# Kernel optimization log

Hardware: AMD Instinct MI355X
Metric: run time of the kernel (lower is better)

Reference implementation:

```python
import jax, jax.numpy as jnp
import numpy as np

NEG = 1e9  # large negative bias used by the original code for masked positions


def setup_inputs() -> dict:
    key = jax.random.key(0)
    k1, k2, k3 = jax.random.split(key, 3)
    B, H, W, Ck, Cv = 8, 64, 64, 64, 128
    return {
        "query": jax.random.normal(k1, (B, H, W, Ck), dtype=jnp.float32),
        "key": jax.random.normal(k2, (B, H, W, Ck), dtype=jnp.float32),
        "value": jax.random.normal(k3, (B, H, W, Cv), dtype=jnp.float32),
    }


def reference(query, key, value):
    B, Hq, Wq, Ck = query.shape
    Cv = value.shape[-1]
    Nq = Hq * Wq                      # query canvas size
    Nk = key.shape[1] * key.shape[2]  # key/value canvas size

    q = query.reshape(B, Nq, Ck)
    k = key.reshape(B, Nk, Ck)
    v = value.reshape(B, Nk, Cv)

    # strictly-causal pixelSNAIL mask: pixel i may attend only to pixels j < i
    allowed = jnp.tril(jnp.ones((Nq, Nk), dtype=query.dtype), k=-1)

    # [B, Nq, Nk] scaled dot-product scores
    scores = jnp.einsum("bqc,bkc->bqk", q, k) / jnp.sqrt(jnp.asarray(Ck, query.dtype))
    scores = scores - NEG * (1.0 - allowed)

    # softmax then redundant re-mask (as in the original module)
    probs = jax.nn.softmax(scores, axis=-1) * allowed

    out = jnp.einsum("bqk,bkv->bqv", probs, v)
    return out.reshape(B, Hq, Wq, Cv)
```

## Files before the change

kernel.cpp:

```cpp
#include <hip/hip_runtime.h>
#include <hip/hip_bf16.h>

typedef unsigned short u16;
typedef unsigned int u32;
typedef __attribute__((ext_vector_type(2))) unsigned int u32x2;
typedef __attribute__((ext_vector_type(4))) unsigned int u32x4;
typedef __attribute__((ext_vector_type(4))) float f32x4;
typedef __attribute__((ext_vector_type(8))) short bf16x8;
typedef __attribute__((ext_vector_type(16))) float f32x16;

__device__ __forceinline__ u32 cvtpk(float lo, float hi) {
    __hip_bfloat162 h = __float22bfloat162_rn(make_float2(lo, hi));
    u32 r; __builtin_memcpy(&r, &h, 4);
    return r;
}
__device__ __forceinline__ int crow(int r, int hl) { return (r & 3) + 8 * (r >> 2) + 4 * hl; }

#define NROW 4096
#define CK 64
#define CV 128
#define BUF 24576
#define VT_OFF 8192
#define SWK(R, o) ((((R) << 7) + (o)) ^ (((R) & 7) << 4))
#define SWVG(R) ((((R) >> 3) & 15) ^ (((R) & 7) << 1))
#define SWV(R, o) ((((R) << 8) + (o)) ^ (SWVG(R) << 4))

__global__ __launch_bounds__(512, 2) void attn_k(const float* __restrict__ Qg,
                                                 const float* __restrict__ Kg,
                                                 const float* __restrict__ Vg,
                                                 float* __restrict__ O) {
    __shared__ __align__(16) u16 smem[2 * BUF];

    int bid = blockIdx.x;
    int bb = bid & 7;
    int u  = bid >> 3;
    int t  = threadIdx.x;
    int w  = t >> 6;
    int lane = t & 63;
    int ql = lane & 31, hl = lane >> 5;
    int qsub = w >> 2;
    int jq   = w & 3;
    int uL = u, uH = 63 - u;
    int rA = ((2 * uL + 1) >> 2) + 1;

    const float* Qp = Qg + (size_t)bb * NROW * CK;
    const float* Kp = Kg + (size_t)bb * NROW * CK;
    const float* Vp = Vg + (size_t)bb * NROW * CV;
    const float qscale = 0.125f * 1.44269504088896f;

    bf16x8 qf[4];
    auto loadQ = [&](int T) {
        const float* qb = Qp + (size_t)((T << 5) + ql) * CK;
#pragma unroll
        for (int kc = 0; kc < 4; kc++) {
            const float* qp = qb + kc * 16 + hl * 8;
            f32x4 a = *(const f32x4*)qp;
            f32x4 b2 = *(const f32x4*)(qp + 4);
            u32x4 qq;
            qq[0] = cvtpk(a[0] * qscale, a[1] * qscale);
            qq[1] = cvtpk(a[2] * qscale, a[3] * qscale);
            qq[2] = cvtpk(b2[0] * qscale, b2[1] * qscale);
            qq[3] = cvtpk(b2[2] * qscale, b2[3] * qscale);
            qf[kc] = __builtin_bit_cast(bf16x8, qq);
        }
    };
    int T_cur = 2 * uL + qsub;
    loadQ(T_cur);

    f32x16 acc[4];
#pragma unroll
    for (int vs = 0; vs < 4; vs++)
#pragma unroll
        for (int r = 0; r < 16; r++) acc[vs][r] = 0.f;
    float l = 0.f;

    int jK = t >> 2, kc4 = t & 3;
    int vg = t & 15, jgrp = t >> 4;
    const float* kSrc = Kp + (size_t)jK * CK + kc4 * 16;
    const float* vSrc = Vp + (size_t)(jgrp * 4) * CV + vg * 8;

    f32x4 kr0, kr1, kr2, kr3;
    f32x4 va0, va1, va2, va3, vb0, vb1, vb2, vb3;
    auto prefetch = [&](int jb) {
        const float* kp = kSrc + (size_t)jb * CK;
        kr0 = *(const f32x4*)kp;       kr1 = *(const f32x4*)(kp + 4);
        kr2 = *(const f32x4*)(kp + 8); kr3 = *(const f32x4*)(kp + 12);
        const float* vp = vSrc + (size_t)jb * CV;
        va0 = *(const f32x4*)vp;            vb0 = *(const f32x4*)(vp + 4);
        va1 = *(const f32x4*)(vp + CV);     vb1 = *(const f32x4*)(vp + CV + 4);
        va2 = *(const f32x4*)(vp + 2 * CV); vb2 = *(const f32x4*)(vp + 2 * CV + 4);
        va3 = *(const f32x4*)(vp + 3 * CV); vb3 = *(const f32x4*)(vp + 3 * CV + 4);
    };
    auto store_tile = [&](int bufo) {
        u32x4 kk0, kk1;
        kk0[0] = cvtpk(kr0[0], kr0[1]); kk0[1] = cvtpk(kr0[2], kr0[3]);
        kk0[2] = cvtpk(kr1[0], kr1[1]); kk0[3] = cvtpk(kr1[2], kr1[3]);
        kk1[0] = cvtpk(kr2[0], kr2[1]); kk1[1] = cvtpk(kr2[2], kr2[3]);
        kk1[2] = cvtpk(kr3[0], kr3[1]); kk1[3] = cvtpk(kr3[2], kr3[3]);
        *(u32x4*)&smem[bufo + (SWK(jK, kc4 * 32) >> 1)]      = kk0;
        *(u32x4*)&smem[bufo + (SWK(jK, kc4 * 32 + 16) >> 1)] = kk1;
#pragma unroll
        for (int x = 0; x < 4; x++) {
            int v = vg * 8 + x;
            u32x2 vv; vv[0] = cvtpk(va0[x], va1[x]); vv[1] = cvtpk(va2[x], va3[x]);
            *(u32x2*)&smem[bufo + VT_OFF + (SWV(v, jgrp * 8) >> 1)] = vv;
        }
#pragma unroll
        for (int x = 0; x < 4; x++) {
            int v = vg * 8 + 4 + x;
            u32x2 vv; vv[0] = cvtpk(vb0[x], vb1[x]); vv[1] = cvtpk(vb2[x], vb3[x]);
            *(u32x2*)&smem[bufo + VT_OFF + (SWV(v, jgrp * 8) >> 1)] = vv;
        }
    };

    auto combine = [&](int scratch, int Tq) {
        float* cm = (float*)(smem + scratch);
        float* lA = cm + 8192;
        float lw = l + __shfl_xor(l, 32);
        if (jq == 0) {
#pragma unroll
            for (int vs = 0; vs < 4; vs++)
#pragma unroll
                for (int r = 0; r < 16; r++)
                    cm[qsub * 4096 + crow(r, hl) * 128 + vs * 32 + ql] = acc[vs][r];
            if (lane < 32) lA[qsub * 32 + lane] = lw;
        }
        __syncthreads();
        if (jq == 1) {
#pragma unroll
            for (int vs = 0; vs < 4; vs++)
#pragma unroll
                for (int r = 0; r < 16; r++)
                    cm[qsub * 4096 + crow(r, hl) * 128 + vs * 32 + ql] += acc[vs][r];
            if (lane < 32) lA[qsub * 32 + lane] += lw;
        }
        __syncthreads();
        if (jq == 2) {
#pragma unroll
            for (int vs = 0; vs < 4; vs++)
#pragma unroll
                for (int r = 0; r < 16; r++)
                    cm[qsub * 4096 + crow(r, hl) * 128 + vs * 32 + ql] += acc[vs][r];
            if (lane < 32) lA[qsub * 32 + lane] += lw;
        }
        __syncthreads();
        if (jq == 3) {
            float ltot = lA[qsub * 32 + ql] + lw;
            float inv = ((Tq << 5) + ql == 0) ? 0.f : 1.f / ltot;
            float inv_r[16];
#pragma unroll
            for (int r = 0; r < 16; r++) inv_r[r] = __shfl(inv, crow(r, hl));
            float* Og = O + ((size_t)bb * NROW + ((size_t)Tq << 5)) * CV;
#pragma unroll
            for (int vs = 0; vs < 4; vs++)
#pragma unroll
                for (int r = 0; r < 16; r++)
                    Og[(size_t)crow(r, hl) * CV + vs * 32 + ql] =
                        (cm[qsub * 4096 + crow(r, hl) * 128 + vs * 32 + ql] + acc[vs][r]) * inv_r[r];
        }
        __syncthreads();
    };

    prefetch(0);

    for (int rr = 0; rr < 33; ++rr) {
        int bufo = (rr & 1) * BUF;
        store_tile(bufo);
        __syncthreads();

        if (rr == rA) {
            combine(((rA - 1) & 1) * BUF, T_cur);
#pragma unroll
            for (int vs = 0; vs < 4; vs++)
#pragma unroll
                for (int r = 0; r < 16; r++) acc[vs][r] = 0.f;
            l = 0.f;
            T_cur = 2 * uH + qsub;
            loadQ(T_cur);
        }

        int tt = (rr < rA) ? rr : rr - rA;
        int jS = 4 * tt + jq;

        {
            int nr = rr + 1;
            int jb = (nr < rA) ? (nr << 7)
                               : ((nr <= 32 ? (nr - rA) : (32 - rA)) << 7);
            prefetch(jb);
        }

        if (jS > T_cur) continue;

        bf16x8 kf0 = *(const bf16x8*)&smem[bufo + (SWK(jq * 32 + ql, 0 * 32 + hl * 16) >> 1)];
        bf16x8 kf1 = *(const bf16x8*)&smem[bufo + (SWK(jq * 32 + ql, 1 * 32 + hl * 16) >> 1)];
        bf16x8 kf2 = *(const bf16x8*)&smem[bufo + (SWK(jq * 32 + ql, 2 * 32 + hl * 16) >> 1)];
        bf16x8 kf3 = *(const bf16x8*)&smem[bufo + (SWK(jq * 32 + ql, 3 * 32 + hl * 16) >> 1)];
        f32x16 S;
#pragma unroll
        for (int r = 0; r < 16; r++) S[r] = 0.f;
        __builtin_amdgcn_s_setprio(1);
        S = __builtin_amdgcn_mfma_f32_32x32x16_bf16(kf0, qf[0], S, 0, 0, 0);
        S = __builtin_amdgcn_mfma_f32_32x32x16_bf16(kf1, qf[1], S, 0, 0, 0);
        S = __builtin_amdgcn_mfma_f32_32x32x16_bf16(kf2, qf[2], S, 0, 0, 0);
        S = __builtin_amdgcn_mfma_f32_32x32x16_bf16(kf3, qf[3], S, 0, 0, 0);
        __builtin_amdgcn_s_setprio(0);

        float P[16];
        bool diag = (jS == T_cur);
#pragma unroll
        for (int r = 0; r < 16; r++) {
            float pr = __builtin_exp2f(S[r]);
            if (diag) pr = (crow(r, hl) >= ql) ? 0.f : pr;
            P[r] = pr;
        }
        {
            float s0 = (P[0] + P[1]) + (P[2] + P[3]);
            float s1 = (P[4] + P[5]) + (P[6] + P[7]);
            float s2 = (P[8] + P[9]) + (P[10] + P[11]);
            float s3 = (P[12] + P[13]) + (P[14] + P[15]);
            l += (s0 + s1) + (s2 + s3);
        }

        u32 A0 = cvtpk(P[0], P[1]),   B0 = cvtpk(P[2], P[3]);
        u32 A1 = cvtpk(P[4], P[5]),   B1 = cvtpk(P[6], P[7]);
        u32 A2 = cvtpk(P[8], P[9]),   B2 = cvtpk(P[10], P[11]);
        u32 A3 = cvtpk(P[12], P[13]), B3 = cvtpk(P[14], P[15]);
        u32 s1 = hl ? A0 : A1, s2 = hl ? B0 : B1;
        u32 s3 = hl ? A2 : A3, s4 = hl ? B2 : B3;
        u32 r1 = (u32)__shfl_xor((int)s1, 32);
        u32 r2 = (u32)__shfl_xor((int)s2, 32);
        u32 r3 = (u32)__shfl_xor((int)s3, 32);
        u32 r4 = (u32)__shfl_xor((int)s4, 32);

        bf16x8 vf0[4], vf1[4];
#pragma unroll
        for (int vs = 0; vs < 4; vs++) {
            vf0[vs] = *(const bf16x8*)&smem[bufo + VT_OFF + (SWV(vs * 32 + ql, jq * 64 + hl * 16) >> 1)];
            vf1[vs] = *(const bf16x8*)&smem[bufo + VT_OFF + (SWV(vs * 32 + ql, jq * 64 + 32 + hl * 16) >> 1)];
        }

        u32x4 w0, w1;
        w0[0] = hl ? r1 : A0; w0[1] = hl ? r2 : B0;
        w0[2] = hl ? A1 : r1; w0[3] = hl ? B1 : r2;
        w1[0] = hl ? r3 : A2; w1[1] = hl ? r4 : B2;
        w1[2] = hl ? A3 : r3; w1[3] = hl ? B3 : r4;
        bf16x8 pa0 = __builtin_bit_cast(bf16x8, w0);
        bf16x8 pa1 = __builtin_bit_cast(bf16x8, w1);

        __builtin_amdgcn_s_setprio(1);
#pragma unroll
        for (int vs = 0; vs < 4; vs++)
            acc[vs] = __builtin_amdgcn_mfma_f32_32x32x16_bf16(pa0, vf0[vs], acc[vs], 0, 0, 0);
#pragma unroll
        for (int vs = 0; vs < 4; vs++)
            acc[vs] = __builtin_amdgcn_mfma_f32_32x32x16_bf16(pa1, vf1[vs], acc[vs], 0, 0, 0);
        __builtin_amdgcn_s_setprio(0);
    }

    __syncthreads();
    combine(0, T_cur);
}

extern "C" void kernel_launch(void* const* d_in, const int* in_sizes, int n_in,
                              void* d_out, int out_size, void* d_ws, size_t ws_size,
                              hipStream_t stream) {
    const float* Q = (const float*)d_in[0];
    const float* K = (const float*)d_in[1];
    const float* V = (const float*)d_in[2];
    float* out = (float*)d_out;
    hipLaunchKernelGGL(attn_k, dim3(256), dim3(512), 0, stream, Q, K, V, out);
}
```

Before: 84.03 us.

## Split paired query tiles into separate blocks with single-buffered LDS

Each block used to handle two query tile-pairs (a low and a mirrored high one) across 33 rounds with double-buffered shared memory. Now each block handles one tile-pair, the grid doubles to 512, and blocks are ordered heaviest-first so long tiles start early. Halving LDS and dropping the mid-loop combine should let more blocks be resident, but the single buffer needs an extra barrier per iteration. The QK^T MFMA chain is also split into two independent accumulators to shorten the dependency chain.

```diff
diff --git a/kernel.cpp b/kernel.cpp
--- a/kernel.cpp
+++ b/kernel.cpp
@@ -19,7 +19,6 @@
 #define NROW 4096
 #define CK 64
 #define CV 128
-#define BUF 24576
 #define VT_OFF 8192
 #define SWK(R, o) ((((R) << 7) + (o)) ^ (((R) & 7) << 4))
 #define SWVG(R) ((((R) >> 3) & 15) ^ (((R) & 7) << 1))
@@ -29,19 +28,20 @@
                                                  const float* __restrict__ Kg,
                                                  const float* __restrict__ Vg,
                                                  float* __restrict__ O) {
-    __shared__ __align__(16) u16 smem[2 * BUF];
+    __shared__ __align__(16) u16 smem[24576];
 
     int bid = blockIdx.x;
-    int bb = bid & 7;
-    int u  = bid >> 3;
-    int t  = threadIdx.x;
-    int w  = t >> 6;
+    int bb  = bid & 7;
+    int idx = bid >> 3;
+    int g   = (idx < 32) ? (63 - idx) : (idx - 32);
+    int t   = threadIdx.x;
+    int w   = t >> 6;
     int lane = t & 63;
     int ql = lane & 31, hl = lane >> 5;
     int qsub = w >> 2;
     int jq   = w & 3;
-    int uL = u, uH = 63 - u;
-    int rA = ((2 * uL + 1) >> 2) + 1;
+    int T_cur = 2 * g + qsub;
+    int NR  = ((2 * g + 1) >> 2) + 1;
 
     const float* Qp = Qg + (size_t)bb * NROW * CK;
     const float* Kp = Kg + (size_t)bb * NROW * CK;
@@ -49,8 +49,8 @@
     const float qscale = 0.125f * 1.44269504088896f;
 
     bf16x8 qf[4];
-    auto loadQ = [&](int T) {
-        const float* qb = Qp + (size_t)((T << 5) + ql) * CK;
+    {
+        const float* qb = Qp + (size_t)((T_cur << 5) + ql) * CK;
 #pragma unroll
         for (int kc = 0; kc < 4; kc++) {
             const float* qp = qb + kc * 16 + hl * 8;
@@ -63,9 +63,7 @@
             qq[3] = cvtpk(b2[2] * qscale, b2[3] * qscale);
             qf[kc] = __builtin_bit_cast(bf16x8, qq);
         }
-    };
-    int T_cur = 2 * uL + qsub;
-    loadQ(T_cur);
+    }
 
     f32x16 acc[4];
 #pragma unroll
@@ -91,125 +89,63 @@
         va2 = *(const f32x4*)(vp + 2 * CV); vb2 = *(const f32x4*)(vp + 2 * CV + 4);
         va3 = *(const f32x4*)(vp + 3 * CV); vb3 = *(const f32x4*)(vp + 3 * CV + 4);
     };
-    auto store_tile = [&](int bufo) {
-        u32x4 kk0, kk1;
-        kk0[0] = cvtpk(kr0[0], kr0[1]); kk0[1] = cvtpk(kr0[2], kr0[3]);
-        kk0[2] = cvtpk(kr1[0], kr1[1]); kk0[3] = cvtpk(kr1[2], kr1[3]);
-        kk1[0] = cvtpk(kr2[0], kr2[1]); kk1[1] = cvtpk(kr2[2], kr2[3]);
-        kk1[2] = cvtpk(kr3[0], kr3[1]); kk1[3] = cvtpk(kr3[2], kr3[3]);
-        *(u32x4*)&smem[bufo + (SWK(jK, kc4 * 32) >> 1)]      = kk0;
-        *(u32x4*)&smem[bufo + (SWK(jK, kc4 * 32 + 16) >> 1)] = kk1;
-#pragma unroll
-        for (int x = 0; x < 4; x++) {
-            int v = vg * 8 + x;
-            u32x2 vv; vv[0] = cvtpk(va0[x], va1[x]); vv[1] = cvtpk(va2[x], va3[x]);
-            *(u32x2*)&smem[bufo + VT_OFF + (SWV(v, jgrp * 8) >> 1)] = vv;
-        }
-#pragma unroll
-        for (int x = 0; x < 4; x++) {
-            int v = vg * 8 + 4 + x;
-            u32x2 vv; vv[0] = cvtpk(vb0[x], vb1[x]); vv[1] = cvtpk(vb2[x], vb3[x]);
-            *(u32x2*)&smem[bufo + VT_OFF + (SWV(v, jgrp * 8) >> 1)] = vv;
-        }
-    };
-
-    auto combine = [&](int scratch, int Tq) {
-        float* cm = (float*)(smem + scratch);
-        float* lA = cm + 8192;
-        float lw = l + __shfl_xor(l, 32);
-        if (jq == 0) {
-#pragma unroll
-            for (int vs = 0; vs < 4; vs++)
-#pragma unroll
-                for (int r = 0; r < 16; r++)
-                    cm[qsub * 4096 + crow(r, hl) * 128 + vs * 32 + ql] = acc[vs][r];
-            if (lane < 32) lA[qsub * 32 + lane] = lw;
-        }
+
+    prefetch(0);
+
+    for (int tt = 0; tt < NR; ++tt) {
         __syncthreads();
-        if (jq == 1) {
-#pragma unroll
-            for (int vs = 0; vs < 4; vs++)
-#pragma unroll
-                for (int r = 0; r < 16; r++)
-                    cm[qsub * 4096 + crow(r, hl) * 128 + vs * 32 + ql] += acc[vs][r];
-            if (lane < 32) lA[qsub * 32 + lane] += lw;
+        {
+            u32x4 kk0, kk1;
+            kk0[0] = cvtpk(kr0[0], kr0[1]); kk0[1] = cvtpk(kr0[2], kr0[3]);
+            kk0[2] = cvtpk(kr1[0], kr1[1]); kk0[3] = cvtpk(kr1[2], kr1[3]);
+            kk1[0] = cvtpk(kr2[0], kr2[1]); kk1[1] = cvtpk(kr2[2], kr2[3]);
+            kk1[2] = cvtpk(kr3[0], kr3[1]); kk1[3] = cvtpk(kr3[2], kr3[3]);
+            *(u32x4*)&smem[SWK(jK, kc4 * 32) >> 1]      = kk0;
+            *(u32x4*)&smem[SWK(jK, kc4 * 32 + 16) >> 1] = kk1;
+#pragma unroll
+            for (int x = 0; x < 4; x++) {
+                int v = vg * 8 + x;
+                u32x2 vv; vv[0] = cvtpk(va0[x], va1[x]); vv[1] = cvtpk(va2[x], va3[x]);
+                *(u32x2*)&smem[VT_OFF + (SWV(v, jgrp * 8) >> 1)] = vv;
+            }
+#pragma unroll
+            for (int x = 0; x < 4; x++) {
+                int v = vg * 8 + 4 + x;
+                u32x2 vv; vv[0] = cvtpk(vb0[x], vb1[x]); vv[1] = cvtpk(vb2[x], vb3[x]);
+                *(u32x2*)&smem[VT_OFF + (SWV(v, jgrp * 8) >> 1)] = vv;
+            }
         }
         __syncthreads();
-        if (jq == 2) {
-#pragma unroll
-            for (int vs = 0; vs < 4; vs++)
-#pragma unroll
-                for (int r = 0; r < 16; r++)
-                    cm[qsub * 4096 + crow(r, hl) * 128 + vs * 32 + ql] += acc[vs][r];
-            if (lane < 32) lA[qsub * 32 + lane] += lw;
-        }
-        __syncthreads();
-        if (jq == 3) {
-            float ltot = lA[qsub * 32 + ql] + lw;
-            float inv = ((Tq << 5) + ql == 0) ? 0.f : 1.f / ltot;
-            float inv_r[16];
-#pragma unroll
-            for (int r = 0; r < 16; r++) inv_r[r] = __shfl(inv, crow(r, hl));
-            float* Og = O + ((size_t)bb * NROW + ((size_t)Tq << 5)) * CV;
-#pragma unroll
-            for (int vs = 0; vs < 4; vs++)
-#pragma unroll
-                for (int r = 0; r < 16; r++)
-                    Og[(size_t)crow(r, hl) * CV + vs * 32 + ql] =
-                        (cm[qsub * 4096 + crow(r, hl) * 128 + vs * 32 + ql] + acc[vs][r]) * inv_r[r];
-        }
-        __syncthreads();
-    };
-
-    prefetch(0);
-
-    for (int rr = 0; rr < 33; ++rr) {
-        int bufo = (rr & 1) * BUF;
-        store_tile(bufo);
-        __syncthreads();
-
-        if (rr == rA) {
-            combine(((rA - 1) & 1) * BUF, T_cur);
-#pragma unroll
-            for (int vs = 0; vs < 4; vs++)
-#pragma unroll
-                for (int r = 0; r < 16; r++) acc[vs][r] = 0.f;
-            l = 0.f;
-            T_cur = 2 * uH + qsub;
-            loadQ(T_cur);
-        }
-
-        int tt = (rr < rA) ? rr : rr - rA;
+
         int jS = 4 * tt + jq;
 
+        bf16x8 kf0 = *(const bf16x8*)&smem[SWK(jq * 32 + ql, 0 * 32 + hl * 16) >> 1];
+        bf16x8 kf1 = *(const bf16x8*)&smem[SWK(jq * 32 + ql, 1 * 32 + hl * 16) >> 1];
+        bf16x8 kf2 = *(const bf16x8*)&smem[SWK(jq * 32 + ql, 2 * 32 + hl * 16) >> 1];
+        bf16x8 kf3 = *(const bf16x8*)&smem[SWK(jq * 32 + ql, 3 * 32 + hl * 16) >> 1];
+
         {
-            int nr = rr + 1;
-            int jb = (nr < rA) ? (nr << 7)
-                               : ((nr <= 32 ? (nr - rA) : (32 - rA)) << 7);
-            prefetch(jb);
+            int nt = (tt + 1 < NR) ? (tt + 1) : tt;
+            prefetch(nt << 7);
         }
 
         if (jS > T_cur) continue;
 
-        bf16x8 kf0 = *(const bf16x8*)&smem[bufo + (SWK(jq * 32 + ql, 0 * 32 + hl * 16) >> 1)];
-        bf16x8 kf1 = *(const bf16x8*)&smem[bufo + (SWK(jq * 32 + ql, 1 * 32 + hl * 16) >> 1)];
-        bf16x8 kf2 = *(const bf16x8*)&smem[bufo + (SWK(jq * 32 + ql, 2 * 32 + hl * 16) >> 1)];
-        bf16x8 kf3 = *(const bf16x8*)&smem[bufo + (SWK(jq * 32 + ql, 3 * 32 + hl * 16) >> 1)];
-        f32x16 S;
-#pragma unroll
-        for (int r = 0; r < 16; r++) S[r] = 0.f;
+        f32x16 Sa, Sb;
+#pragma unroll
+        for (int r = 0; r < 16; r++) { Sa[r] = 0.f; Sb[r] = 0.f; }
         __builtin_amdgcn_s_setprio(1);
-        S = __builtin_amdgcn_mfma_f32_32x32x16_bf16(kf0, qf[0], S, 0, 0, 0);
-        S = __builtin_amdgcn_mfma_f32_32x32x16_bf16(kf1, qf[1], S, 0, 0, 0);
-        S = __builtin_amdgcn_mfma_f32_32x32x16_bf16(kf2, qf[2], S, 0, 0, 0);
-        S = __builtin_amdgcn_mfma_f32_32x32x16_bf16(kf3, qf[3], S, 0, 0, 0);
+        Sa = __builtin_amdgcn_mfma_f32_32x32x16_bf16(kf0, qf[0], Sa, 0, 0, 0);
+        Sb = __builtin_amdgcn_mfma_f32_32x32x16_bf16(kf2, qf[2], Sb, 0, 0, 0);
+        Sa = __builtin_amdgcn_mfma_f32_32x32x16_bf16(kf1, qf[1], Sa, 0, 0, 0);
+        Sb = __builtin_amdgcn_mfma_f32_32x32x16_bf16(kf3, qf[3], Sb, 0, 0, 0);
         __builtin_amdgcn_s_setprio(0);
 
         float P[16];
         bool diag = (jS == T_cur);
 #pragma unroll
         for (int r = 0; r < 16; r++) {
-            float pr = __builtin_exp2f(S[r]);
+            float pr = __builtin_exp2f(Sa[r] + Sb[r]);
             if (diag) pr = (crow(r, hl) >= ql) ? 0.f : pr;
             P[r] = pr;
         }
@@ -235,8 +171,8 @@
         bf16x8 vf0[4], vf1[4];
 #pragma unroll
         for (int vs = 0; vs < 4; vs++) {
-            vf0[vs] = *(const bf16x8*)&smem[bufo + VT_OFF + (SWV(vs * 32 + ql, jq * 64 + hl * 16) >> 1)];
-            vf1[vs] = *(const bf16x8*)&smem[bufo + VT_OFF + (SWV(vs * 32 + ql, jq * 64 + 32 + hl * 16) >> 1)];
+            vf0[vs] = *(const bf16x8*)&smem[VT_OFF + (SWV(vs * 32 + ql, jq * 64 + hl * 16) >> 1)];
+            vf1[vs] = *(const bf16x8*)&smem[VT_OFF + (SWV(vs * 32 + ql, jq * 64 + 32 + hl * 16) >> 1)];
         }
 
         u32x4 w0, w1;
@@ -258,7 +194,50 @@
     }
 
     __syncthreads();
-    combine(0, T_cur);
+    float* cm = (float*)smem;
+    float* lA = cm + 8192;
+    float lw = l + __shfl_xor(l, 32);
+    if (jq == 0) {
+#pragma unroll
+        for (int vs = 0; vs < 4; vs++)
+#pragma unroll
+            for (int r = 0; r < 16; r++)
+                cm[qsub * 4096 + crow(r, hl) * 128 + vs * 32 + ql] = acc[vs][r];
+        if (lane < 32) lA[qsub * 32 + lane] = lw;
+    }
+    __syncthreads();
+    if (jq == 1) {
+#pragma unroll
+        for (int vs = 0; vs < 4; vs++)
+#pragma unroll
+            for (int r = 0; r < 16; r++)
+                cm[qsub * 4096 + crow(r, hl) * 128 + vs * 32 + ql] += acc[vs][r];
+        if (lane < 32) lA[qsub * 32 + lane] += lw;
+    }
+    __syncthreads();
+    if (jq == 2) {
+#pragma unroll
+        for (int vs = 0; vs < 4; vs++)
+#pragma unroll
+            for (int r = 0; r < 16; r++)
+                cm[qsub * 4096 + crow(r, hl) * 128 + vs * 32 + ql] += acc[vs][r];
+        if (lane < 32) lA[qsub * 32 + lane] += lw;
+    }
+    __syncthreads();
+    if (jq == 3) {
+        float ltot = lA[qsub * 32 + ql] + lw;
+        float inv = ((T_cur << 5) + ql == 0) ? 0.f : 1.f / ltot;
+        float inv_r[16];
+#pragma unroll
+        for (int r = 0; r < 16; r++) inv_r[r] = __shfl(inv, crow(r, hl));
+        float* Og = O + ((size_t)bb * NROW + ((size_t)T_cur << 5)) * CV;
+#pragma unroll
+        for (int vs = 0; vs < 4; vs++)
+#pragma unroll
+            for (int r = 0; r < 16; r++)
+                Og[(size_t)crow(r, hl) * CV + vs * 32 + ql] =
+                    (cm[qsub * 4096 + crow(r, hl) * 128 + vs * 32 + ql] + acc[vs][r]) * inv_r[r];
+    }
 }
 
 extern "C" void kernel_launch(void* const* d_in, const int* in_sizes, int n_in,
@@ -268,5 +247,5 @@
     const float* K = (const float*)d_in[1];
     const float* V = (const float*)d_in[2];
     float* out = (float*)d_out;
-    hipLaunchKernelGGL(attn_k, dim3(256), dim3(512), 0, stream, Q, K, V, out);
+    hipLaunchKernelGGL(attn_k, dim3(512), dim3(512), 0, stream, Q, K, V, out);
 }
```

Measured after the change: 104.2 us. 1.24x slower.

## Pre-convert K/V to swizzled bf16 tiles and stream them via global_load_lds

Applied to the files above, without the earlier changes.

A prep kernel converts K and V to bf16 and writes them into workspace already in the swizzled shared-memory tile layout. The main kernel then copies each tile straight into LDS with async global_load_lds double buffering, removing per-block fp32 loads, conversions and LDS stores that every query block previously repeated. The cost is an extra kernel launch and a workspace round trip. The combine step moves to a dedicated scratch region, which enlarges the LDS footprint. The old path is kept as a fallback when the workspace is too small.

```diff
diff --git a/kernel.cpp b/kernel.cpp
--- a/kernel.cpp
+++ b/kernel.cpp
@@ -9,6 +9,9 @@
 typedef __attribute__((ext_vector_type(8))) short bf16x8;
 typedef __attribute__((ext_vector_type(16))) float f32x16;
 
+typedef __attribute__((address_space(1))) const void as1_cvoid;
+typedef __attribute__((address_space(3))) void as3_void;
+
 __device__ __forceinline__ u32 cvtpk(float lo, float hi) {
     __hip_bfloat162 h = __float22bfloat162_rn(make_float2(lo, hi));
     u32 r; __builtin_memcpy(&r, &h, 4);
@@ -19,17 +22,57 @@
 #define NROW 4096
 #define CK 64
 #define CV 128
-#define BUF 24576
-#define VT_OFF 8192
+#define TILE_U16 24576
+#define WS_NEEDED (8u * 32u * 49152u)
 #define SWK(R, o) ((((R) << 7) + (o)) ^ (((R) & 7) << 4))
 #define SWVG(R) ((((R) >> 3) & 15) ^ (((R) & 7) << 1))
 #define SWV(R, o) ((((R) << 8) + (o)) ^ (SWVG(R) << 4))
 
-__global__ __launch_bounds__(512, 2) void attn_k(const float* __restrict__ Qg,
-                                                 const float* __restrict__ Kg,
+__global__ __launch_bounds__(512, 2) void prep_k(const float* __restrict__ Kg,
                                                  const float* __restrict__ Vg,
+                                                 u16* __restrict__ ws) {
+    int bid = blockIdx.x;
+    int b = bid >> 5, jt = bid & 31;
+    int t = threadIdx.x;
+    int jK = t >> 2, kc4 = t & 3;
+    int vg = t & 15, jgrp = t >> 4;
+    const float* Kp = Kg + ((size_t)b * NROW + jt * 128) * CK;
+    const float* Vp = Vg + ((size_t)b * NROW + jt * 128) * CV;
+    u16* img = ws + (size_t)(b * 32 + jt) * TILE_U16;
+
+    {
+        const float* kp = Kp + (size_t)jK * CK + kc4 * 16;
+        f32x4 a0 = *(const f32x4*)kp,       a1 = *(const f32x4*)(kp + 4);
+        f32x4 a2 = *(const f32x4*)(kp + 8), a3 = *(const f32x4*)(kp + 12);
+        u32x4 kk0, kk1;
+        kk0[0] = cvtpk(a0[0], a0[1]); kk0[1] = cvtpk(a0[2], a0[3]);
+        kk0[2] = cvtpk(a1[0], a1[1]); kk0[3] = cvtpk(a1[2], a1[3]);
+        kk1[0] = cvtpk(a2[0], a2[1]); kk1[1] = cvtpk(a2[2], a2[3]);
+        kk1[2] = cvtpk(a3[0], a3[1]); kk1[3] = cvtpk(a3[2], a3[3]);
+        *(u32x4*)&img[SWK(jK, kc4 * 32) >> 1]      = kk0;
+        *(u32x4*)&img[SWK(jK, kc4 * 32 + 16) >> 1] = kk1;
+    }
+    {
+        const float* vp = Vp + (size_t)(jgrp * 4) * CV + vg * 8;
+        f32x4 va0 = *(const f32x4*)vp,            vb0 = *(const f32x4*)(vp + 4);
+        f32x4 va1 = *(const f32x4*)(vp + CV),     vb1 = *(const f32x4*)(vp + CV + 4);
+        f32x4 va2 = *(const f32x4*)(vp + 2 * CV), vb2 = *(const f32x4*)(vp + 2 * CV + 4);
+        f32x4 va3 = *(const f32x4*)(vp + 3 * CV), vb3 = *(const f32x4*)(vp + 3 * CV + 4);
+#pragma unroll
+        for (int x = 0; x < 4; x++) {
+            u32x2 vv;
+            vv[0] = cvtpk(va0[x], va1[x]); vv[1] = cvtpk(va2[x], va3[x]);
+            *(u32x2*)&img[8192 + (SWV(vg * 8 + x, jgrp * 8) >> 1)] = vv;
+            vv[0] = cvtpk(vb0[x], vb1[x]); vv[1] = cvtpk(vb2[x], vb3[x]);
+            *(u32x2*)&img[8192 + (SWV(vg * 8 + 4 + x, jgrp * 8) >> 1)] = vv;
+        }
+    }
+}
+
+__global__ __launch_bounds__(512, 2) void attn_m(const float* __restrict__ Qg,
+                                                 const u16* __restrict__ ws,
                                                  float* __restrict__ O) {
-    __shared__ __align__(16) u16 smem[2 * BUF];
+    __shared__ __align__(16) u16 smem[2 * TILE_U16 + 16512];
 
     int bid = blockIdx.x;
     int bb = bid & 7;
@@ -41,11 +84,11 @@
     int qsub = w >> 2;
     int jq   = w & 3;
     int uL = u, uH = 63 - u;
-    int rA = ((2 * uL + 1) >> 2) + 1;
+    int NR1 = ((2 * uL + 1) >> 2) + 1;
+    int NR2 = 33 - NR1;
 
     const float* Qp = Qg + (size_t)bb * NROW * CK;
-    const float* Kp = Kg + (size_t)bb * NROW * CK;
-    const float* Vp = Vg + (size_t)bb * NROW * CV;
+    const u16* imgB = ws + (size_t)bb * 32 * TILE_U16;
     const float qscale = 0.125f * 1.44269504088896f;
 
     bf16x8 qf[4];
@@ -74,13 +117,213 @@
         for (int r = 0; r < 16; r++) acc[vs][r] = 0.f;
     float l = 0.f;
 
+    auto issueTile = [&](int img_tile, int buf_u16) {
+        const char* src = (const char*)(imgB + (size_t)img_tile * TILE_U16)
+                          + w * 6144 + lane * 16;
+        char* dst = (char*)smem + (size_t)buf_u16 * 2 + w * 6144;
+#pragma unroll
+        for (int i = 0; i < 6; i++)
+            __builtin_amdgcn_global_load_lds((as1_cvoid*)(src + i * 1024),
+                                             (as3_void*)(dst + i * 1024), 16, 0, 0);
+    };
+
+    auto combine = [&](int Tq) {
+        float* cm = (float*)&smem[2 * TILE_U16];
+        float* lA = cm + 8192;
+        float lw = l + __shfl_xor(l, 32);
+        if (jq == 0) {
+#pragma unroll
+            for (int vs = 0; vs < 4; vs++)
+#pragma unroll
+                for (int r = 0; r < 16; r++)
+                    cm[qsub * 4096 + crow(r, hl) * 128 + vs * 32 + ql] = acc[vs][r];
+            if (lane < 32) lA[qsub * 32 + lane] = lw;
+        }
+        __syncthreads();
+        if (jq == 1) {
+#pragma unroll
+            for (int vs = 0; vs < 4; vs++)
+#pragma unroll
+                for (int r = 0; r < 16; r++)
+                    cm[qsub * 4096 + crow(r, hl) * 128 + vs * 32 + ql] += acc[vs][r];
+            if (lane < 32) lA[qsub * 32 + lane] += lw;
+        }
+        __syncthreads();
+        if (jq == 2) {
+#pragma unroll
+            for (int vs = 0; vs < 4; vs++)
+#pragma unroll
+                for (int r = 0; r < 16; r++)
+                    cm[qsub * 4096 + crow(r, hl) * 128 + vs * 32 + ql] += acc[vs][r];
+            if (lane < 32) lA[qsub * 32 + lane] += lw;
+        }
+        __syncthreads();
+        if (jq == 3) {
+            float ltot = lA[qsub * 32 + ql] + lw;
+            float inv = ((Tq << 5) + ql == 0) ? 0.f : 1.f / ltot;
+            float inv_r[16];
+#pragma unroll
+            for (int r = 0; r < 16; r++) inv_r[r] = __shfl(inv, crow(r, hl));
+            float* Og = O + ((size_t)bb * NROW + ((size_t)Tq << 5)) * CV;
+#pragma unroll
+            for (int vs = 0; vs < 4; vs++)
+#pragma unroll
+                for (int r = 0; r < 16; r++)
+                    Og[(size_t)crow(r, hl) * CV + vs * 32 + ql] =
+                        (cm[qsub * 4096 + crow(r, hl) * 128 + vs * 32 + ql] + acc[vs][r]) * inv_r[r];
+        }
+        __syncthreads();
+    };
+
+    issueTile(0, 0);
+
+    for (int rr = 0; rr < 33; ++rr) {
+        int cur = (rr & 1) * TILE_U16;
+        int nxt = ((rr + 1) & 1) * TILE_U16;
+
+        {
+            int nr = rr + 1;
+            int jb = (nr < NR1) ? nr : (nr - NR1 < NR2 ? nr - NR1 : NR2 - 1);
+            issueTile(jb, nxt);
+        }
+        asm volatile("s_waitcnt vmcnt(6)" ::: "memory");
+        __syncthreads();
+
+        if (rr == NR1) {
+            combine(T_cur);
+#pragma unroll
+            for (int vs = 0; vs < 4; vs++)
+#pragma unroll
+                for (int r = 0; r < 16; r++) acc[vs][r] = 0.f;
+            l = 0.f;
+            T_cur = 2 * uH + qsub;
+            loadQ(T_cur);
+        }
+
+        int tt = (rr < NR1) ? rr : rr - NR1;
+        int jS = 4 * tt + jq;
+        if (jS <= T_cur) {
+            bf16x8 kf0 = *(const bf16x8*)&smem[cur + (SWK(jq * 32 + ql, 0 * 32 + hl * 16) >> 1)];
+            bf16x8 kf1 = *(const bf16x8*)&smem[cur + (SWK(jq * 32 + ql, 1 * 32 + hl * 16) >> 1)];
+            bf16x8 kf2 = *(const bf16x8*)&smem[cur + (SWK(jq * 32 + ql, 2 * 32 + hl * 16) >> 1)];
+            bf16x8 kf3 = *(const bf16x8*)&smem[cur + (SWK(jq * 32 + ql, 3 * 32 + hl * 16) >> 1)];
+
+            f32x16 S;
+#pragma unroll
+            for (int r = 0; r < 16; r++) S[r] = 0.f;
+            __builtin_amdgcn_s_setprio(1);
+            S = __builtin_amdgcn_mfma_f32_32x32x16_bf16(kf0, qf[0], S, 0, 0, 0);
+            S = __builtin_amdgcn_mfma_f32_32x32x16_bf16(kf1, qf[1], S, 0, 0, 0);
+            S = __builtin_amdgcn_mfma_f32_32x32x16_bf16(kf2, qf[2], S, 0, 0, 0);
+            S = __builtin_amdgcn_mfma_f32_32x32x16_bf16(kf3, qf[3], S, 0, 0, 0);
+            __builtin_amdgcn_s_setprio(0);
+
+            float P[16];
+            bool diag = (jS == T_cur);
+#pragma unroll
+            for (int r = 0; r < 16; r++) {
+                float pr2 = __builtin_exp2f(S[r]);
+                if (diag) pr2 = (crow(r, hl) >= ql) ? 0.f : pr2;
+                P[r] = pr2;
+            }
+            {
+                float s0 = (P[0] + P[1]) + (P[2] + P[3]);
+                float s1 = (P[4] + P[5]) + (P[6] + P[7]);
+                float s2 = (P[8] + P[9]) + (P[10] + P[11]);
+                float s3 = (P[12] + P[13]) + (P[14] + P[15]);
+                l += (s0 + s1) + (s2 + s3);
+            }
+
+            u32 A0 = cvtpk(P[0], P[1]),   B0 = cvtpk(P[2], P[3]);
+            u32 A1 = cvtpk(P[4], P[5]),   B1 = cvtpk(P[6], P[7]);
+            u32 A2 = cvtpk(P[8], P[9]),   B2 = cvtpk(P[10], P[11]);
+            u32 A3 = cvtpk(P[12], P[13]), B3 = cvtpk(P[14], P[15]);
+            u32 s1 = hl ? A0 : A1, s2 = hl ? B0 : B1;
+            u32 s3 = hl ? A2 : A3, s4 = hl ? B2 : B3;
+            u32 r1 = (u32)__shfl_xor((int)s1, 32);
+            u32 r2 = (u32)__shfl_xor((int)s2, 32);
+            u32 r3 = (u32)__shfl_xor((int)s3, 32);
+            u32 r4 = (u32)__shfl_xor((int)s4, 32);
+
+            bf16x8 vf0[4], vf1[4];
+#pragma unroll
+            for (int vs = 0; vs < 4; vs++) {
+                vf0[vs] = *(const bf16x8*)&smem[cur + 8192 + (SWV(vs * 32 + ql, jq * 64 + hl * 16) >> 1)];
+                vf1[vs] = *(const bf16x8*)&smem[cur + 8192 + (SWV(vs * 32 + ql, jq * 64 + 32 + hl * 16) >> 1)];
+            }
+            u32x4 w0, w1;
+            w0[0] = hl ? r1 : A0; w0[1] = hl ? r2 : B0;
+            w0[2] = hl ? A1 : r1; w0[3] = hl ? B1 : r2;
+            w1[0] = hl ? r3 : A2; w1[1] = hl ? r4 : B2;
+            w1[2] = hl ? A3 : r3; w1[3] = hl ? B3 : r4;
+            bf16x8 pa0 = __builtin_bit_cast(bf16x8, w0);
+            bf16x8 pa1 = __builtin_bit_cast(bf16x8, w1);
+
+            __builtin_amdgcn_s_setprio(1);
+#pragma unroll
+            for (int vs = 0; vs < 4; vs++)
+                acc[vs] = __builtin_amdgcn_mfma_f32_32x32x16_bf16(pa0, vf0[vs], acc[vs], 0, 0, 0);
+#pragma unroll
+            for (int vs = 0; vs < 4; vs++)
+                acc[vs] = __builtin_amdgcn_mfma_f32_32x32x16_bf16(pa1, vf1[vs], acc[vs], 0, 0, 0);
+            __builtin_amdgcn_s_setprio(0);
+        }
+        __syncthreads();
+    }
+
+    combine(T_cur);
+}
+
+#define FBUF 24576
+#define FVT 8192
+__global__ __launch_bounds__(512, 2) void attn_fb(const float* __restrict__ Qg,
+                                                  const float* __restrict__ Kg,
+                                                  const float* __restrict__ Vg,
+                                                  float* __restrict__ O) {
+    __shared__ __align__(16) u16 smem[2 * FBUF];
+    int bid = blockIdx.x;
+    int bb = bid & 7;
+    int u  = bid >> 3;
+    int t  = threadIdx.x;
+    int w  = t >> 6;
+    int lane = t & 63;
+    int ql = lane & 31, hl = lane >> 5;
+    int qsub = w >> 2, jq = w & 3;
+    int uL = u, uH = 63 - u;
+    int rA = ((2 * uL + 1) >> 2) + 1;
+    const float* Qp = Qg + (size_t)bb * NROW * CK;
+    const float* Kp = Kg + (size_t)bb * NROW * CK;
+    const float* Vp = Vg + (size_t)bb * NROW * CV;
+    const float qscale = 0.125f * 1.44269504088896f;
+    bf16x8 qf[4];
+    auto loadQ = [&](int T) {
+        const float* qb = Qp + (size_t)((T << 5) + ql) * CK;
+#pragma unroll
+        for (int kc = 0; kc < 4; kc++) {
+            const float* qp = qb + kc * 16 + hl * 8;
+            f32x4 a = *(const f32x4*)qp;
+            f32x4 b2 = *(const f32x4*)(qp + 4);
+            u32x4 qq;
+            qq[0] = cvtpk(a[0] * qscale, a[1] * qscale);
+            qq[1] = cvtpk(a[2] * qscale, a[3] * qscale);
+            qq[2] = cvtpk(b2[0] * qscale, b2[1] * qscale);
+            qq[3] = cvtpk(b2[2] * qscale, b2[3] * qscale);
+            qf[kc] = __builtin_bit_cast(bf16x8, qq);
+        }
+    };
+    int T_cur = 2 * uL + qsub;
+    loadQ(T_cur);
+    f32x16 acc[4];
+#pragma unroll
+    for (int vs = 0; vs < 4; vs++)
+#pragma unroll
+        for (int r = 0; r < 16; r++) acc[vs][r] = 0.f;
+    float l = 0.f;
     int jK = t >> 2, kc4 = t & 3;
     int vg = t & 15, jgrp = t >> 4;
     const float* kSrc = Kp + (size_t)jK * CK + kc4 * 16;
     const float* vSrc = Vp + (size_t)(jgrp * 4) * CV + vg * 8;
-
-    f32x4 kr0, kr1, kr2, kr3;
-    f32x4 va0, va1, va2, va3, vb0, vb1, vb2, vb3;
+    f32x4 kr0, kr1, kr2, kr3, va0, va1, va2, va3, vb0, vb1, vb2, vb3;
     auto prefetch = [&](int jb) {
         const float* kp = kSrc + (size_t)jb * CK;
         kr0 = *(const f32x4*)kp;       kr1 = *(const f32x4*)(kp + 4);
@@ -103,16 +346,15 @@
         for (int x = 0; x < 4; x++) {
             int v = vg * 8 + x;
             u32x2 vv; vv[0] = cvtpk(va0[x], va1[x]); vv[1] = cvtpk(va2[x], va3[x]);
-            *(u32x2*)&smem[bufo + VT_OFF + (SWV(v, jgrp * 8) >> 1)] = vv;
+            *(u32x2*)&smem[bufo + FVT + (SWV(v, jgrp * 8) >> 1)] = vv;
         }
 #pragma unroll
         for (int x = 0; x < 4; x++) {
             int v = vg * 8 + 4 + x;
             u32x2 vv; vv[0] = cvtpk(vb0[x], vb1[x]); vv[1] = cvtpk(vb2[x], vb3[x]);
-            *(u32x2*)&smem[bufo + VT_OFF + (SWV(v, jgrp * 8) >> 1)] = vv;
-        }
-    };
-
+            *(u32x2*)&smem[bufo + FVT + (SWV(v, jgrp * 8) >> 1)] = vv;
+        }
+    };
     auto combine = [&](int scratch, int Tq) {
         float* cm = (float*)(smem + scratch);
         float* lA = cm + 8192;
@@ -160,16 +402,13 @@
         }
         __syncthreads();
     };
-
     prefetch(0);
-
     for (int rr = 0; rr < 33; ++rr) {
-        int bufo = (rr & 1) * BUF;
+        int bufo = (rr & 1) * FBUF;
         store_tile(bufo);
         __syncthreads();
-
         if (rr == rA) {
-            combine(((rA - 1) & 1) * BUF, T_cur);
+            combine(((rA - 1) & 1) * FBUF, T_cur);
 #pragma unroll
             for (int vs = 0; vs < 4; vs++)
 #pragma unroll
@@ -178,19 +417,15 @@
             T_cur = 2 * uH + qsub;
             loadQ(T_cur);
         }
-
         int tt = (rr < rA) ? rr : rr - rA;
         int jS = 4 * tt + jq;
-
         {
             int nr = rr + 1;
             int jb = (nr < rA) ? (nr << 7)
                                : ((nr <= 32 ? (nr - rA) : (32 - rA)) << 7);
             prefetch(jb);
         }
-
         if (jS > T_cur) continue;
-
         bf16x8 kf0 = *(const bf16x8*)&smem[bufo + (SWK(jq * 32 + ql, 0 * 32 + hl * 16) >> 1)];
         bf16x8 kf1 = *(const bf16x8*)&smem[bufo + (SWK(jq * 32 + ql, 1 * 32 + hl * 16) >> 1)];
         bf16x8 kf2 = *(const bf16x8*)&smem[bufo + (SWK(jq * 32 + ql, 2 * 32 + hl * 16) >> 1)];
@@ -204,14 +439,13 @@
         S = __builtin_amdgcn_mfma_f32_32x32x16_bf16(kf2, qf[2], S, 0, 0, 0);
         S = __builtin_amdgcn_mfma_f32_32x32x16_bf16(kf3, qf[3], S, 0, 0, 0);
         __builtin_amdgcn_s_setprio(0);
-
         float P[16];
         bool diag = (jS == T_cur);
 #pragma unroll
         for (int r = 0; r < 16; r++) {
-            float pr = __builtin_exp2f(S[r]);
-            if (diag) pr = (crow(r, hl) >= ql) ? 0.f : pr;
-            P[r] = pr;
+            float pr2 = __builtin_exp2f(S[r]);
+            if (diag) pr2 = (crow(r, hl) >= ql) ? 0.f : pr2;
+            P[r] = pr2;
         }
         {
             float s0 = (P[0] + P[1]) + (P[2] + P[3]);
@@ -220,7 +454,6 @@
             float s3 = (P[12] + P[13]) + (P[14] + P[15]);
             l += (s0 + s1) + (s2 + s3);
         }
-
         u32 A0 = cvtpk(P[0], P[1]),   B0 = cvtpk(P[2], P[3]);
         u32 A1 = cvtpk(P[4], P[5]),   B1 = cvtpk(P[6], P[7]);
         u32 A2 = cvtpk(P[8], P[9]),   B2 = cvtpk(P[10], P[11]);
@@ -231,14 +464,12 @@
         u32 r2 = (u32)__shfl_xor((int)s2, 32);
         u32 r3 = (u32)__shfl_xor((int)s3, 32);
         u32 r4 = (u32)__shfl_xor((int)s4, 32);
-
         bf16x8 vf0[4], vf1[4];
 #pragma unroll
         for (int vs = 0; vs < 4; vs++) {
-            vf0[vs] = *(const bf16x8*)&smem[bufo + VT_OFF + (SWV(vs * 32 + ql, jq * 64 + hl * 16) >> 1)];
-            vf1[vs] = *(const bf16x8*)&smem[bufo + VT_OFF + (SWV(vs * 32 + ql, jq * 64 + 32 + hl * 16) >> 1)];
-        }
-
+            vf0[vs] = *(const bf16x8*)&smem[bufo + FVT + (SWV(vs * 32 + ql, jq * 64 + hl * 16) >> 1)];
+            vf1[vs] = *(const bf16x8*)&smem[bufo + FVT + (SWV(vs * 32 + ql, jq * 64 + 32 + hl * 16) >> 1)];
+        }
         u32x4 w0, w1;
         w0[0] = hl ? r1 : A0; w0[1] = hl ? r2 : B0;
         w0[2] = hl ? A1 : r1; w0[3] = hl ? B1 : r2;
@@ -246,7 +477,6 @@
         w1[2] = hl ? A3 : r3; w1[3] = hl ? B3 : r4;
         bf16x8 pa0 = __builtin_bit_cast(bf16x8, w0);
         bf16x8 pa1 = __builtin_bit_cast(bf16x8, w1);
-
         __builtin_amdgcn_s_setprio(1);
 #pragma unroll
         for (int vs = 0; vs < 4; vs++)
@@ -256,7 +486,6 @@
             acc[vs] = __builtin_amdgcn_mfma_f32_32x32x16_bf16(pa1, vf1[vs], acc[vs], 0, 0, 0);
         __builtin_amdgcn_s_setprio(0);
     }
-
     __syncthreads();
     combine(0, T_cur);
 }
@@ -268,5 +497,11 @@
     const float* K = (const float*)d_in[1];
     const float* V = (const float*)d_in[2];
     float* out = (float*)d_out;
-    hipLaunchKernelGGL(attn_k, dim3(256), dim3(512), 0, stream, Q, K, V, out);
+    if (ws_size >= (size_t)WS_NEEDED) {
+        u16* ws = (u16*)d_ws;
+        hipLaunchKernelGGL(prep_k, dim3(256), dim3(512), 0, stream, K, V, ws);
+        hipLaunchKernelGGL(attn_m, dim3(256), dim3(512), 0, stream, Q, ws, out);
+    } else {
+        hipLaunchKernelGGL(attn_fb, dim3(256), dim3(512), 0, stream, Q, K, V, out);
+    }
 }
```

New measurement: 81.63 us. 1.03x faster.
